# Optimization experiments

Hardware: AMD Instinct MI355X
Metric: run time of the kernel (lower is better)

The kernel has to match this reference:

```python
import jax, jax.numpy as jnp
import numpy as np

# SRU cell math (sru library v2.x, has_skip_term=False, identity activation):
#   U = x @ W  ->  split into (u0, u1, u2), each [L, B, H]
#   f_t = sigmoid(u1_t + v_f * c_{t-1} + b_f)
#   r_t = sigmoid(u2_t + v_r * c_{t-1} + b_r)
#   c_t = f_t * c_{t-1} + (1 - f_t) * u0_t
#   h_t = r_t * c_t            (no skip term, identity activation)

L, B, D, H, OUT = 512, 128, 128, 512, 5


def sru_layer(x, W, vc, b):
    # x: [L, B, Din]; W: [Din, 3H]; vc: [2H]; b: [2H]
    h = W.shape[1] // 3
    U = jnp.einsum('lbd,dk->lbk', x, W)          # [L, B, 3H]
    u0, u1, u2 = jnp.split(U, 3, axis=-1)
    vf, vr = vc[:h], vc[h:]
    bf, br = b[:h], b[h:]

    def step(c, u):
        u0t, u1t, u2t = u
        f = jax.nn.sigmoid(u1t + vf * c + bf)
        r = jax.nn.sigmoid(u2t + vr * c + br)
        c_new = f * c + (1.0 - f) * u0t
        return c_new, r * c_new

    c0 = jnp.zeros((x.shape[1], h), dtype=x.dtype)
    _, hs = jax.lax.scan(step, c0, (u0, u1, u2))  # hs: [L, B, H]
    return hs


def setup_inputs() -> dict:
    key = jax.random.key(0)
    ks = jax.random.split(key, 9)
    s_in = 1.0 / np.sqrt(D)
    s_h = 1.0 / np.sqrt(H)
    return {
        'x': jax.random.normal(ks[0], (L, B, D), jnp.float32),
        'W0': jax.random.normal(ks[1], (D, 3 * H), jnp.float32) * s_in,
        'v0': jax.random.normal(ks[2], (2 * H,), jnp.float32) * s_h,
        'b0': jnp.zeros((2 * H,), jnp.float32),
        'W1': jax.random.normal(ks[3], (H, 3 * H), jnp.float32) * s_h,
        'v1': jax.random.normal(ks[4], (2 * H,), jnp.float32) * s_h,
        'b1': jnp.zeros((2 * H,), jnp.float32),
        'fc_w': jax.random.normal(ks[5], (OUT, H), jnp.float32) * s_h,
        'fc_b': jnp.zeros((OUT,), jnp.float32),
    }


def reference(x, W0, v0, b0, W1, v1, b1, fc_w, fc_b):
    h1 = sru_layer(x, W0, v0, b0)    # [L, B, H]
    h2 = sru_layer(h1, W1, v1, b1)   # [L, B, H]
    # fc on last timestep
    return h2[-1] @ fc_w.T + fc_b    # [B, OUT]
```

## Files before the change

kernel.cpp:

```cpp
#include <hip/hip_runtime.h>
#include <math.h>

#define L_SEQ 512
#define BATCH 128
#define DIN   128
#define HID   512
#define NOUT  5

typedef unsigned short u16;
typedef unsigned int   u32;
typedef __attribute__((ext_vector_type(8))) short short8;
typedef __attribute__((ext_vector_type(4))) float f32x4;

__device__ __forceinline__ u16 f2bf(float x) {
  u32 u = __float_as_uint(x);
  return (u16)((u + 0x7fffu + ((u >> 16) & 1u)) >> 16);
}
__device__ __forceinline__ float bf2f(u16 s) {
  return __uint_as_float(((u32)s) << 16);
}
__device__ __forceinline__ void gload16(const void* g, void* l) {
  __builtin_amdgcn_global_load_lds(
      (const __attribute__((address_space(1))) u32*)g,
      (__attribute__((address_space(3))) u32*)l, 16, 0, 0);
}

#define R_AH 0
#define R_AL 8192
#define R_BH 16384
#define R_BL 20480
#define BUFSZ 24576u

__global__ __launch_bounds__(512, 1)
void gemm_bf16x3_8ph(const u16* __restrict__ Ah, const u16* __restrict__ Al,
                     const u16* __restrict__ Bh, const u16* __restrict__ Bl,
                     float* __restrict__ C, int N, int K, int NBX) {
  __shared__ u16 lds[3 * BUFSZ];

  const int NT = K >> 5;
  const int nwg = gridDim.x;
  int bid = blockIdx.x;
  if ((nwg & 7) == 0) {
    const int cpx = nwg >> 3;
    bid = (bid & 7) * cpx + (bid >> 3);
  }
  const int bx = bid % NBX, by = bid / NBX;

  const int tid = threadIdx.x;
  const int w = tid >> 6, lane = tid & 63;

  const int srow = lane >> 2;
  const int sslot = lane & 3;
  const int ra0 = w * 16 + srow;
  const int ra1 = 128 + ra0;
  const int swA0 = sslot ^ ((ra0 >> 1) & 3);
  const int swA1 = sslot ^ ((ra1 >> 1) & 3);
  const u16* pAh0 = Ah + (size_t)(by * 256 + ra0) * K + swA0 * 8;
  const u16* pAh1 = Ah + (size_t)(by * 256 + ra1) * K + swA1 * 8;
  const u16* pAl0 = Al + (size_t)(by * 256 + ra0) * K + swA0 * 8;
  const u16* pAl1 = Al + (size_t)(by * 256 + ra1) * K + swA1 * 8;
  const u16* pBh0 = Bh + (size_t)(bx * 128 + ra0) * K + swA0 * 8;
  const u16* pBl0 = Bl + (size_t)(bx * 128 + ra0) * K + swA0 * 8;
  const int dA0 = (w * 16) * 32;
  const int dA1 = (128 + w * 16) * 32;

  const int wm = w >> 1, wn = w & 1;
  const int frow = lane & 15, fsl = lane >> 4;
  int offA[4], offB[4];
#pragma unroll
  for (int i = 0; i < 4; ++i) {
    const int ra = wm * 64 + i * 16 + frow;
    offA[i] = ra * 32 + ((fsl ^ ((ra >> 1) & 3)) * 8);
    const int rb = wn * 64 + i * 16 + frow;
    offB[i] = rb * 32 + ((fsl ^ ((rb >> 1) & 3)) * 8);
  }

  f32x4 acc[4][4];
#pragma unroll
  for (int i = 0; i < 4; ++i)
#pragma unroll
    for (int j = 0; j < 4; ++j)
#pragma unroll
      for (int q = 0; q < 4; ++q) acc[i][j][q] = 0.f;

#define STAGE_A0(ks, stg) do { \
    gload16(pAh0 + (ks), &lds[(stg) + R_AH + dA0]); \
    gload16(pAl0 + (ks), &lds[(stg) + R_AL + dA0]); } while (0)
#define STAGE_A1(ks, stg) do { \
    gload16(pAh1 + (ks), &lds[(stg) + R_AH + dA1]); \
    gload16(pAl1 + (ks), &lds[(stg) + R_AL + dA1]); } while (0)
#define STAGE_BH(ks, stg) gload16(pBh0 + (ks), &lds[(stg) + R_BH + dA0])
#define STAGE_BL(ks, stg) gload16(pBl0 + (ks), &lds[(stg) + R_BL + dA0])

  STAGE_A0(0, 0u); STAGE_A1(0, 0u); STAGE_BH(0, 0u); STAGE_BL(0, 0u);
  STAGE_A0(32, BUFSZ); STAGE_A1(32, BUFSZ); STAGE_BH(32, BUFSZ); STAGE_BL(32, BUFSZ);
  asm volatile("s_waitcnt vmcnt(6)" ::: "memory");
  __builtin_amdgcn_s_barrier();

  unsigned bufs0 = 0, bufs1 = BUFSZ, bufs2 = 2 * BUFSZ;

#define PHASE(i, STAGE_STMT, TAIL) do { \
    const short8 a_h = *(const short8*)&lds[bufs0 + R_AH + offA[i]]; \
    const short8 a_l = *(const short8*)&lds[bufs0 + R_AL + offA[i]]; \
    STAGE_STMT; \
    __builtin_amdgcn_s_barrier(); \
    asm volatile("s_waitcnt lgkmcnt(0)" ::: "memory"); \
    __builtin_amdgcn_sched_barrier(0); \
    __builtin_amdgcn_s_setprio(1); \
    _Pragma("unroll") \
    for (int j = 0; j < 4; ++j) { \
      acc[i][j] = __builtin_amdgcn_mfma_f32_16x16x32_bf16(a_h, bh[j], acc[i][j], 0, 0, 0); \
      acc[i][j] = __builtin_amdgcn_mfma_f32_16x16x32_bf16(a_h, bl[j], acc[i][j], 0, 0, 0); \
      acc[i][j] = __builtin_amdgcn_mfma_f32_16x16x32_bf16(a_l, bh[j], acc[i][j], 0, 0, 0); \
    } \
    __builtin_amdgcn_s_setprio(0); \
    TAIL; \
    __builtin_amdgcn_s_barrier(); \
  } while (0)

  for (int t = 0; t < NT; ++t) {
    const int ks = (t + 2) * 32;
    const bool st = (t + 2) < NT;

    short8 bh[4], bl[4];
#pragma unroll
    for (int j = 0; j < 4; ++j) {
      bh[j] = *(const short8*)&lds[bufs0 + R_BH + offB[j]];
      bl[j] = *(const short8*)&lds[bufs0 + R_BL + offB[j]];
    }
    PHASE(0, if (st) STAGE_A0(ks, bufs2), );
    PHASE(1, if (st) STAGE_A1(ks, bufs2), );
    PHASE(2, if (st) STAGE_BH(ks, bufs2), );
    PHASE(3, if (st) STAGE_BL(ks, bufs2),
          if (t < NT - 2) { asm volatile("s_waitcnt vmcnt(6)" ::: "memory"); }
          else if (t == NT - 2) { asm volatile("s_waitcnt vmcnt(0)" ::: "memory"); });

    const unsigned tmp = bufs0; bufs0 = bufs1; bufs1 = bufs2; bufs2 = tmp;
  }
#undef PHASE
#undef STAGE_A0
#undef STAGE_A1
#undef STAGE_BH
#undef STAGE_BL

  const int crow0 = by * 256 + wm * 64 + (lane >> 4) * 4;
  const int ccol0 = bx * 128 + wn * 64 + (lane & 15);
#pragma unroll
  for (int i = 0; i < 4; ++i)
#pragma unroll
    for (int j = 0; j < 4; ++j) {
      float* cp = C + (size_t)(crow0 + i * 16) * N + ccol0 + j * 16;
#pragma unroll
      for (int q = 0; q < 4; ++q) cp[(size_t)q * N] = acc[i][j][q];
    }
}

__global__ __launch_bounds__(256)
void split4_f32(const float* __restrict__ in, u16* __restrict__ hi,
                u16* __restrict__ lo, int n4) {
  const int i = blockIdx.x * 256 + threadIdx.x;
  if (i >= n4) return;
  const float4 v = ((const float4*)in)[i];
  u16 h0 = f2bf(v.x), h1 = f2bf(v.y), h2 = f2bf(v.z), h3 = f2bf(v.w);
  u16 l0 = f2bf(v.x - bf2f(h0)), l1 = f2bf(v.y - bf2f(h1));
  u16 l2 = f2bf(v.z - bf2f(h2)), l3 = f2bf(v.w - bf2f(h3));
  uint2 hp, lp;
  hp.x = (u32)h0 | ((u32)h1 << 16); hp.y = (u32)h2 | ((u32)h3 << 16);
  lp.x = (u32)l0 | ((u32)l1 << 16); lp.y = (u32)l2 | ((u32)l3 << 16);
  ((uint2*)hi)[i] = hp;
  ((uint2*)lo)[i] = lp;
}

__global__ __launch_bounds__(256)
void split_w_t(const float* __restrict__ W, u16* __restrict__ Th,
               u16* __restrict__ Tl, int K, int N) {
  const int idx = blockIdx.x * 256 + threadIdx.x;
  if (idx >= K * N) return;
  const int k = idx / N, n = idx - k * N;
  const float x = W[idx];
  const u16 h = f2bf(x);
  Th[(size_t)n * K + k] = h;
  Tl[(size_t)n * K + k] = f2bf(x - bf2f(h));
}

__global__ __launch_bounds__(256)
void zero_f32(float* __restrict__ p, int n) {
  const int i = blockIdx.x * 256 + threadIdx.x;
  if (i < n) p[i] = 0.f;
}

__device__ __forceinline__ float sig(float x) { return 1.f / (1.f + __expf(-x)); }

__global__ __launch_bounds__(256)
void sru_scan0_chunk(const float* __restrict__ U, const float* __restrict__ v,
                     const float* __restrict__ bias, u16* __restrict__ h1h,
                     u16* __restrict__ h1l, float* __restrict__ cstate, int Tc) {
  const int j = blockIdx.x * 256 + threadIdx.x;
  const int b = j >> 9, h = j & (HID - 1);
  const float vf = v[h], vr = v[HID + h];
  const float bf = bias[h], br = bias[HID + h];

  const float* p = U + (size_t)b * (3 * HID) + h;
  const size_t sT = (size_t)BATCH * 3 * HID;
  u16* ph = h1h + (size_t)b * HID + h;
  u16* pl = h1l + (size_t)b * HID + h;
  const size_t sH = (size_t)BATCH * HID;

  float c = cstate[j];
  float cu[12];
#pragma unroll
  for (int q = 0; q < 4; ++q) {
    cu[3 * q + 0] = p[q * sT];
    cu[3 * q + 1] = p[q * sT + HID];
    cu[3 * q + 2] = p[q * sT + 2 * HID];
  }
  const int NG = Tc >> 2;
  for (int g = 0; g < NG; ++g) {
    float nx[12];
    const bool has = (g + 1 < NG);
    if (has) {
      const float* pn = p + 4 * sT;
#pragma unroll
      for (int q = 0; q < 4; ++q) {
        nx[3 * q + 0] = pn[q * sT];
        nx[3 * q + 1] = pn[q * sT + HID];
        nx[3 * q + 2] = pn[q * sT + 2 * HID];
      }
    }
#pragma unroll
    for (int q = 0; q < 4; ++q) {
      const float u0 = cu[3 * q], u1 = cu[3 * q + 1], u2 = cu[3 * q + 2];
      const float f = sig(u1 + vf * c + bf);
      const float r = sig(u2 + vr * c + br);
      c = f * c + (1.f - f) * u0;
      const float hv = r * c;
      const u16 hh = f2bf(hv);
      ph[(size_t)(g * 4 + q) * sH] = hh;
      pl[(size_t)(g * 4 + q) * sH] = f2bf(hv - bf2f(hh));
    }
    p += 4 * sT;
    if (has) {
#pragma unroll
      for (int i = 0; i < 12; ++i) cu[i] = nx[i];
    }
  }
  cstate[j] = c;
}

__global__ __launch_bounds__(256)
void sru_scan1_chunk(const float* __restrict__ U, const float* __restrict__ v,
                     const float* __restrict__ bias, float* __restrict__ cstate,
                     float* __restrict__ hlast, int Tc, int lastT) {
  const int j = blockIdx.x * 256 + threadIdx.x;
  const int b = j >> 9, h = j & (HID - 1);
  const float vf = v[h], vr = v[HID + h];
  const float bf = bias[h], br = bias[HID + h];

  const float* p = U + (size_t)b * (3 * HID) + h;
  const size_t sT = (size_t)BATCH * 3 * HID;

  float c = cstate[j];
  float cu[8];
#pragma unroll
  for (int q = 0; q < 4; ++q) {
    cu[2 * q + 0] = p[q * sT];
    cu[2 * q + 1] = p[q * sT + HID];
  }
  const int NG = Tc >> 2;
  for (int g = 0; g < NG; ++g) {
    float nx[8];
    const bool has = (g + 1 < NG);
    if (has) {
      const float* pn = p + 4 * sT;
#pragma unroll
      for (int q = 0; q < 4; ++q) {
        nx[2 * q + 0] = pn[q * sT];
        nx[2 * q + 1] = pn[q * sT + HID];
      }
    }
#pragma unroll
    for (int q = 0; q < 4; ++q) {
      const float u0 = cu[2 * q], u1 = cu[2 * q + 1];
      const float f = sig(u1 + vf * c + bf);
      const float cn = f * c + (1.f - f) * u0;
      if (g * 4 + q == lastT) {
        const float u2 = p[q * sT + 2 * HID];
        const float r = sig(u2 + vr * c + br);
        hlast[j] = r * cn;
      }
      c = cn;
    }
    p += 4 * sT;
    if (has) {
#pragma unroll
      for (int i = 0; i < 8; ++i) cu[i] = nx[i];
    }
  }
  cstate[j] = c;
}

__global__ __launch_bounds__(256)
void fc_head(const float* __restrict__ h, const float* __restrict__ w,
             const float* __restrict__ bias, float* __restrict__ out) {
  const int gid = blockIdx.x * 256 + threadIdx.x;
  const int wv = gid >> 6, lane = threadIdx.x & 63;
  if (wv >= BATCH * NOUT) return;
  const int b = wv / NOUT, o = wv % NOUT;
  float s = 0.f;
#pragma unroll
  for (int k = lane; k < HID; k += 64)
    s += h[(size_t)b * HID + k] * w[(size_t)o * HID + k];
#pragma unroll
  for (int off = 32; off > 0; off >>= 1) s += __shfl_down(s, off);
  if (lane == 0) out[(size_t)b * NOUT + o] = s + bias[o];
}

extern "C" void kernel_launch(void* const* d_in, const int* in_sizes, int n_in,
                              void* d_out, int out_size, void* d_ws, size_t ws_size,
                              hipStream_t stream) {
  const float* x   = (const float*)d_in[0];
  const float* W0  = (const float*)d_in[1];
  const float* v0  = (const float*)d_in[2];
  const float* b0  = (const float*)d_in[3];
  const float* W1  = (const float*)d_in[4];
  const float* v1  = (const float*)d_in[5];
  const float* b1  = (const float*)d_in[6];
  const float* fcw = (const float*)d_in[7];
  const float* fcb = (const float*)d_in[8];
  float* out = (float*)d_out;

  const size_t nX = (size_t)L_SEQ * BATCH * DIN;
  const size_t nW0 = (size_t)DIN * 3 * HID;
  const size_t nW1 = (size_t)HID * 3 * HID;

  int Tc = 128;
  for (;;) {
    size_t f32e = (size_t)Tc * BATCH * 3 * HID + 3 * (size_t)BATCH * HID;
    size_t u16e = 2 * nX + 2 * (size_t)Tc * BATCH * HID + 2 * nW0 + 2 * nW1;
    if (f32e * 4 + u16e * 2 + 1024 <= ws_size || Tc <= 8) break;
    Tc >>= 1;
  }
  const int NC = L_SEQ / Tc;
  const int Mc = Tc * BATCH;

  float* U0c = (float*)d_ws;
  float* c0  = U0c + (size_t)Mc * 3 * HID;
  float* c1  = c0 + (size_t)BATCH * HID;
  float* h2  = c1 + (size_t)BATCH * HID;
  u16* xs_h  = (u16*)(h2 + (size_t)BATCH * HID);
  u16* xs_l  = xs_h + nX;
  u16* h1_h  = xs_l + nX;
  u16* h1_l  = h1_h + (size_t)Mc * HID;
  u16* w0t_h = h1_l + (size_t)Mc * HID;
  u16* w0t_l = w0t_h + nW0;
  u16* w1t_h = w0t_l + nW0;
  u16* w1t_l = w1t_h + nW1;

  const int scan_grid = (BATCH * HID) / 256;
  const int fc_grid = (BATCH * NOUT * 64 + 255) / 256;
  const int grid_full = (Mc / 256) * 12;
  const int grid_01   = (Mc / 256) * 8;

  zero_f32<<<(2 * BATCH * HID) / 256, 256, 0, stream>>>(c0, 2 * BATCH * HID);
  split4_f32<<<(int)(nX / 4 + 255) / 256, 256, 0, stream>>>(x, xs_h, xs_l, (int)(nX / 4));
  split_w_t<<<(int)(nW0 + 255) / 256, 256, 0, stream>>>(W0, w0t_h, w0t_l, DIN, 3 * HID);
  split_w_t<<<(int)(nW1 + 255) / 256, 256, 0, stream>>>(W1, w1t_h, w1t_l, HID, 3 * HID);

  for (int ch = 0; ch < NC; ++ch) {
    const bool last = (ch == NC - 1);
    const size_t xoff = (size_t)ch * Tc * BATCH * DIN;
    gemm_bf16x3_8ph<<<grid_full, 512, 0, stream>>>(
        xs_h + xoff, xs_l + xoff, w0t_h, w0t_l, U0c, 3 * HID, DIN, 12);
    sru_scan0_chunk<<<scan_grid, 256, 0, stream>>>(U0c, v0, b0, h1_h, h1_l, c0, Tc);
    gemm_bf16x3_8ph<<<last ? grid_full : grid_01, 512, 0, stream>>>(
        h1_h, h1_l, w1t_h, w1t_l, U0c, 3 * HID, HID, last ? 12 : 8);
    sru_scan1_chunk<<<scan_grid, 256, 0, stream>>>(
        U0c, v1, b1, c1, h2, Tc, last ? Tc - 1 : -1);
  }
  fc_head<<<fc_grid, 256, 0, stream>>>(h2, fcw, fcb, out);
}
```

Baseline: 712.5 us.

## Enlarge GEMM tile to 256x256 with double-buffered LDS and drop zero kernel

Rewrites the split-bf16 GEMM to compute 256x256 output tiles per workgroup instead of 256x128. Each wave now holds an 8x4 accumulator block, and the kernel uses a two-stage LDS buffer in place of three stages. The larger tile halves the grid and raises operand reuse per loaded byte. In exchange it costs more accumulator registers (launch bounds now ask for 2 blocks) and gives a shallower prefetch pipeline. The separate zero-init kernel is also removed: the scan kernels now start from c=0 on the first chunk through a flag.

```diff
diff --git a/kernel.cpp b/kernel.cpp
--- a/kernel.cpp
+++ b/kernel.cpp
@@ -25,17 +25,13 @@
       (__attribute__((address_space(3))) u32*)l, 16, 0, 0);
 }
 
-#define R_AH 0
-#define R_AL 8192
-#define R_BH 16384
-#define R_BL 20480
-#define BUFSZ 24576u
-
-__global__ __launch_bounds__(512, 1)
-void gemm_bf16x3_8ph(const u16* __restrict__ Ah, const u16* __restrict__ Al,
-                     const u16* __restrict__ Bh, const u16* __restrict__ Bl,
-                     float* __restrict__ C, int N, int K, int NBX) {
-  __shared__ u16 lds[3 * BUFSZ];
+#define BUFSZ 32768u
+
+__global__ __launch_bounds__(512, 2)
+void gemm_bf16x3_v2(const u16* __restrict__ Ah, const u16* __restrict__ Al,
+                    const u16* __restrict__ Bh, const u16* __restrict__ Bl,
+                    float* __restrict__ C, int N, int K, int NBX) {
+  __shared__ u16 lds[2 * BUFSZ];
 
   const int NT = K >> 5;
   const int nwg = gridDim.x;
@@ -48,105 +44,126 @@
 
   const int tid = threadIdx.x;
   const int w = tid >> 6, lane = tid & 63;
-
-  const int srow = lane >> 2;
-  const int sslot = lane & 3;
-  const int ra0 = w * 16 + srow;
-  const int ra1 = 128 + ra0;
-  const int swA0 = sslot ^ ((ra0 >> 1) & 3);
-  const int swA1 = sslot ^ ((ra1 >> 1) & 3);
-  const u16* pAh0 = Ah + (size_t)(by * 256 + ra0) * K + swA0 * 8;
-  const u16* pAh1 = Ah + (size_t)(by * 256 + ra1) * K + swA1 * 8;
-  const u16* pAl0 = Al + (size_t)(by * 256 + ra0) * K + swA0 * 8;
-  const u16* pAl1 = Al + (size_t)(by * 256 + ra1) * K + swA1 * 8;
-  const u16* pBh0 = Bh + (size_t)(bx * 128 + ra0) * K + swA0 * 8;
-  const u16* pBl0 = Bl + (size_t)(bx * 128 + ra0) * K + swA0 * 8;
-  const int dA0 = (w * 16) * 32;
-  const int dA1 = (128 + w * 16) * 32;
-
-  const int wm = w >> 1, wn = w & 1;
+  const int wm = w >> 2, wn = w & 3;
+
+  const int r16 = lane >> 2, sl = lane & 3;
+  const int bB0 = wn * 64 + wm * 32;
+  const int aB0 = wm * 128 + wn * 16;
+
+  const int rB0 = bB0 + r16,      rB1 = bB0 + 16 + r16;
+  const int rA0 = aB0 + r16,      rA1 = aB0 + 64 + r16;
+  const u16* pB0h = Bh + (size_t)(bx * 256 + rB0) * K + ((sl ^ ((rB0 >> 1) & 3)) * 8);
+  const u16* pB0l = Bl + (size_t)(bx * 256 + rB0) * K + ((sl ^ ((rB0 >> 1) & 3)) * 8);
+  const u16* pB1h = Bh + (size_t)(bx * 256 + rB1) * K + ((sl ^ ((rB1 >> 1) & 3)) * 8);
+  const u16* pB1l = Bl + (size_t)(bx * 256 + rB1) * K + ((sl ^ ((rB1 >> 1) & 3)) * 8);
+  const u16* pA0h = Ah + (size_t)(by * 256 + rA0) * K + ((sl ^ ((rA0 >> 1) & 3)) * 8);
+  const u16* pA0l = Al + (size_t)(by * 256 + rA0) * K + ((sl ^ ((rA0 >> 1) & 3)) * 8);
+  const u16* pA1h = Ah + (size_t)(by * 256 + rA1) * K + ((sl ^ ((rA1 >> 1) & 3)) * 8);
+  const u16* pA1l = Al + (size_t)(by * 256 + rA1) * K + ((sl ^ ((rA1 >> 1) & 3)) * 8);
+  const int dB = 16384 + bB0 * 32;
+  const int dA = aB0 * 32;
+
+#define STAGE_P0(ks, sb) do { gload16(pB0h + (ks), &lds[(sb) + dB]); \
+                              gload16(pB0l + (ks), &lds[(sb) + dB + 8192]); } while (0)
+#define STAGE_P1(ks, sb) do { gload16(pB1h + (ks), &lds[(sb) + dB + 512]); \
+                              gload16(pB1l + (ks), &lds[(sb) + dB + 8704]); } while (0)
+#define STAGE_P2(ks, sb) do { gload16(pA0h + (ks), &lds[(sb) + dA]); \
+                              gload16(pA0l + (ks), &lds[(sb) + dA + 8192]); } while (0)
+#define STAGE_P3(ks, sb) do { gload16(pA1h + (ks), &lds[(sb) + dA + 2048]); \
+                              gload16(pA1l + (ks), &lds[(sb) + dA + 10240]); } while (0)
+
   const int frow = lane & 15, fsl = lane >> 4;
-  int offA[4], offB[4];
-#pragma unroll
-  for (int i = 0; i < 4; ++i) {
-    const int ra = wm * 64 + i * 16 + frow;
+  int offA[8], offB[4];
+#pragma unroll
+  for (int i = 0; i < 8; ++i) {
+    const int ra = wm * 128 + i * 16 + frow;
     offA[i] = ra * 32 + ((fsl ^ ((ra >> 1) & 3)) * 8);
-    const int rb = wn * 64 + i * 16 + frow;
-    offB[i] = rb * 32 + ((fsl ^ ((rb >> 1) & 3)) * 8);
-  }
-
-  f32x4 acc[4][4];
-#pragma unroll
-  for (int i = 0; i < 4; ++i)
+  }
+#pragma unroll
+  for (int j = 0; j < 4; ++j) {
+    const int rb = wn * 64 + j * 16 + frow;
+    offB[j] = 16384 + rb * 32 + ((fsl ^ ((rb >> 1) & 3)) * 8);
+  }
+
+  f32x4 acc[8][4];
+#pragma unroll
+  for (int i = 0; i < 8; ++i)
 #pragma unroll
     for (int j = 0; j < 4; ++j)
 #pragma unroll
       for (int q = 0; q < 4; ++q) acc[i][j][q] = 0.f;
 
-#define STAGE_A0(ks, stg) do { \
-    gload16(pAh0 + (ks), &lds[(stg) + R_AH + dA0]); \
-    gload16(pAl0 + (ks), &lds[(stg) + R_AL + dA0]); } while (0)
-#define STAGE_A1(ks, stg) do { \
-    gload16(pAh1 + (ks), &lds[(stg) + R_AH + dA1]); \
-    gload16(pAl1 + (ks), &lds[(stg) + R_AL + dA1]); } while (0)
-#define STAGE_BH(ks, stg) gload16(pBh0 + (ks), &lds[(stg) + R_BH + dA0])
-#define STAGE_BL(ks, stg) gload16(pBl0 + (ks), &lds[(stg) + R_BL + dA0])
-
-  STAGE_A0(0, 0u); STAGE_A1(0, 0u); STAGE_BH(0, 0u); STAGE_BL(0, 0u);
-  STAGE_A0(32, BUFSZ); STAGE_A1(32, BUFSZ); STAGE_BH(32, BUFSZ); STAGE_BL(32, BUFSZ);
-  asm volatile("s_waitcnt vmcnt(6)" ::: "memory");
+  STAGE_P0(0, 0u); STAGE_P1(0, 0u); STAGE_P2(0, 0u); STAGE_P3(0, 0u);
+  asm volatile("s_waitcnt vmcnt(0)" ::: "memory");
   __builtin_amdgcn_s_barrier();
 
-  unsigned bufs0 = 0, bufs1 = BUFSZ, bufs2 = 2 * BUFSZ;
-
-#define PHASE(i, STAGE_STMT, TAIL) do { \
-    const short8 a_h = *(const short8*)&lds[bufs0 + R_AH + offA[i]]; \
-    const short8 a_l = *(const short8*)&lds[bufs0 + R_AL + offA[i]]; \
-    STAGE_STMT; \
+#define MFMA3(i, j, aa_h, aa_l) \
+    acc[i][j] = __builtin_amdgcn_mfma_f32_16x16x32_bf16(aa_h, bh[j], acc[i][j], 0, 0, 0); \
+    acc[i][j] = __builtin_amdgcn_mfma_f32_16x16x32_bf16(aa_h, bl[j], acc[i][j], 0, 0, 0); \
+    acc[i][j] = __builtin_amdgcn_mfma_f32_16x16x32_bf16(aa_l, bh[j], acc[i][j], 0, 0, 0)
+
+#define PHASE(p, STG, TAIL) do { \
+    const short8 ah0 = *(const short8*)&lds[cb + offA[2 * (p)]]; \
+    const short8 al0 = *(const short8*)&lds[cb + 8192 + offA[2 * (p)]]; \
+    const short8 ah1 = *(const short8*)&lds[cb + offA[2 * (p) + 1]]; \
+    const short8 al1 = *(const short8*)&lds[cb + 8192 + offA[2 * (p) + 1]]; \
+    STG; \
     __builtin_amdgcn_s_barrier(); \
     asm volatile("s_waitcnt lgkmcnt(0)" ::: "memory"); \
     __builtin_amdgcn_sched_barrier(0); \
     __builtin_amdgcn_s_setprio(1); \
     _Pragma("unroll") \
     for (int j = 0; j < 4; ++j) { \
-      acc[i][j] = __builtin_amdgcn_mfma_f32_16x16x32_bf16(a_h, bh[j], acc[i][j], 0, 0, 0); \
-      acc[i][j] = __builtin_amdgcn_mfma_f32_16x16x32_bf16(a_h, bl[j], acc[i][j], 0, 0, 0); \
-      acc[i][j] = __builtin_amdgcn_mfma_f32_16x16x32_bf16(a_l, bh[j], acc[i][j], 0, 0, 0); \
+      acc[2*(p)][j]   = __builtin_amdgcn_mfma_f32_16x16x32_bf16(ah0, bh[j], acc[2*(p)][j], 0, 0, 0); \
+      acc[2*(p)+1][j] = __builtin_amdgcn_mfma_f32_16x16x32_bf16(ah1, bh[j], acc[2*(p)+1][j], 0, 0, 0); \
+    } \
+    _Pragma("unroll") \
+    for (int j = 0; j < 4; ++j) { \
+      acc[2*(p)][j]   = __builtin_amdgcn_mfma_f32_16x16x32_bf16(ah0, bl[j], acc[2*(p)][j], 0, 0, 0); \
+      acc[2*(p)+1][j] = __builtin_amdgcn_mfma_f32_16x16x32_bf16(ah1, bl[j], acc[2*(p)+1][j], 0, 0, 0); \
+    } \
+    _Pragma("unroll") \
+    for (int j = 0; j < 4; ++j) { \
+      acc[2*(p)][j]   = __builtin_amdgcn_mfma_f32_16x16x32_bf16(al0, bh[j], acc[2*(p)][j], 0, 0, 0); \
+      acc[2*(p)+1][j] = __builtin_amdgcn_mfma_f32_16x16x32_bf16(al1, bh[j], acc[2*(p)+1][j], 0, 0, 0); \
     } \
     __builtin_amdgcn_s_setprio(0); \
     TAIL; \
     __builtin_amdgcn_s_barrier(); \
   } while (0)
 
+  int cb = 0;
   for (int t = 0; t < NT; ++t) {
-    const int ks = (t + 2) * 32;
-    const bool st = (t + 2) < NT;
+    const int ks = (t + 1) << 5;
+    const bool st = (t + 1) < NT;
+    const int sb = cb ^ (int)BUFSZ;
 
     short8 bh[4], bl[4];
 #pragma unroll
     for (int j = 0; j < 4; ++j) {
-      bh[j] = *(const short8*)&lds[bufs0 + R_BH + offB[j]];
-      bl[j] = *(const short8*)&lds[bufs0 + R_BL + offB[j]];
-    }
-    PHASE(0, if (st) STAGE_A0(ks, bufs2), );
-    PHASE(1, if (st) STAGE_A1(ks, bufs2), );
-    PHASE(2, if (st) STAGE_BH(ks, bufs2), );
-    PHASE(3, if (st) STAGE_BL(ks, bufs2),
-          if (t < NT - 2) { asm volatile("s_waitcnt vmcnt(6)" ::: "memory"); }
-          else if (t == NT - 2) { asm volatile("s_waitcnt vmcnt(0)" ::: "memory"); });
-
-    const unsigned tmp = bufs0; bufs0 = bufs1; bufs1 = bufs2; bufs2 = tmp;
+      bh[j] = *(const short8*)&lds[cb + offB[j]];
+      bl[j] = *(const short8*)&lds[cb + 8192 + offB[j]];
+    }
+    PHASE(0, if (st) STAGE_P0(ks, sb), );
+    PHASE(1, if (st) STAGE_P1(ks, sb),
+          if (st) { asm volatile("s_waitcnt vmcnt(4)" ::: "memory"); }
+          else    { asm volatile("s_waitcnt vmcnt(0)" ::: "memory"); });
+    PHASE(2, if (st) STAGE_P2(ks, sb), );
+    PHASE(3, if (st) STAGE_P3(ks, sb),
+          if (st) { asm volatile("s_waitcnt vmcnt(2)" ::: "memory"); });
+    cb = sb;
   }
 #undef PHASE
-#undef STAGE_A0
-#undef STAGE_A1
-#undef STAGE_BH
-#undef STAGE_BL
-
-  const int crow0 = by * 256 + wm * 64 + (lane >> 4) * 4;
-  const int ccol0 = bx * 128 + wn * 64 + (lane & 15);
-#pragma unroll
-  for (int i = 0; i < 4; ++i)
+#undef MFMA3
+#undef STAGE_P0
+#undef STAGE_P1
+#undef STAGE_P2
+#undef STAGE_P3
+
+  const int crow0 = by * 256 + wm * 128 + (lane >> 4) * 4;
+  const int ccol0 = bx * 256 + wn * 64 + (lane & 15);
+#pragma unroll
+  for (int i = 0; i < 8; ++i)
 #pragma unroll
     for (int j = 0; j < 4; ++j) {
       float* cp = C + (size_t)(crow0 + i * 16) * N + ccol0 + j * 16;
@@ -183,18 +200,13 @@
   Tl[(size_t)n * K + k] = f2bf(x - bf2f(h));
 }
 
-__global__ __launch_bounds__(256)
-void zero_f32(float* __restrict__ p, int n) {
-  const int i = blockIdx.x * 256 + threadIdx.x;
-  if (i < n) p[i] = 0.f;
-}
-
 __device__ __forceinline__ float sig(float x) { return 1.f / (1.f + __expf(-x)); }
 
 __global__ __launch_bounds__(256)
 void sru_scan0_chunk(const float* __restrict__ U, const float* __restrict__ v,
                      const float* __restrict__ bias, u16* __restrict__ h1h,
-                     u16* __restrict__ h1l, float* __restrict__ cstate, int Tc) {
+                     u16* __restrict__ h1l, float* __restrict__ cstate, int Tc,
+                     int init) {
   const int j = blockIdx.x * 256 + threadIdx.x;
   const int b = j >> 9, h = j & (HID - 1);
   const float vf = v[h], vr = v[HID + h];
@@ -206,7 +218,7 @@
   u16* pl = h1l + (size_t)b * HID + h;
   const size_t sH = (size_t)BATCH * HID;
 
-  float c = cstate[j];
+  float c = init ? 0.f : cstate[j];
   float cu[12];
 #pragma unroll
   for (int q = 0; q < 4; ++q) {
@@ -250,7 +262,7 @@
 __global__ __launch_bounds__(256)
 void sru_scan1_chunk(const float* __restrict__ U, const float* __restrict__ v,
                      const float* __restrict__ bias, float* __restrict__ cstate,
-                     float* __restrict__ hlast, int Tc, int lastT) {
+                     float* __restrict__ hlast, int Tc, int lastT, int init) {
   const int j = blockIdx.x * 256 + threadIdx.x;
   const int b = j >> 9, h = j & (HID - 1);
   const float vf = v[h], vr = v[HID + h];
@@ -259,7 +271,7 @@
   const float* p = U + (size_t)b * (3 * HID) + h;
   const size_t sT = (size_t)BATCH * 3 * HID;
 
-  float c = cstate[j];
+  float c = init ? 0.f : cstate[j];
   float cu[8];
 #pragma unroll
   for (int q = 0; q < 4; ++q) {
@@ -358,10 +370,9 @@
 
   const int scan_grid = (BATCH * HID) / 256;
   const int fc_grid = (BATCH * NOUT * 64 + 255) / 256;
-  const int grid_full = (Mc / 256) * 12;
-  const int grid_01   = (Mc / 256) * 8;
-
-  zero_f32<<<(2 * BATCH * HID) / 256, 256, 0, stream>>>(c0, 2 * BATCH * HID);
+  const int grid_full = (Mc / 256) * 6;
+  const int grid_01   = (Mc / 256) * 4;
+
   split4_f32<<<(int)(nX / 4 + 255) / 256, 256, 0, stream>>>(x, xs_h, xs_l, (int)(nX / 4));
   split_w_t<<<(int)(nW0 + 255) / 256, 256, 0, stream>>>(W0, w0t_h, w0t_l, DIN, 3 * HID);
   split_w_t<<<(int)(nW1 + 255) / 256, 256, 0, stream>>>(W1, w1t_h, w1t_l, HID, 3 * HID);
@@ -369,13 +380,14 @@
   for (int ch = 0; ch < NC; ++ch) {
     const bool last = (ch == NC - 1);
     const size_t xoff = (size_t)ch * Tc * BATCH * DIN;
-    gemm_bf16x3_8ph<<<grid_full, 512, 0, stream>>>(
-        xs_h + xoff, xs_l + xoff, w0t_h, w0t_l, U0c, 3 * HID, DIN, 12);
-    sru_scan0_chunk<<<scan_grid, 256, 0, stream>>>(U0c, v0, b0, h1_h, h1_l, c0, Tc);
-    gemm_bf16x3_8ph<<<last ? grid_full : grid_01, 512, 0, stream>>>(
-        h1_h, h1_l, w1t_h, w1t_l, U0c, 3 * HID, HID, last ? 12 : 8);
+    gemm_bf16x3_v2<<<grid_full, 512, 0, stream>>>(
+        xs_h + xoff, xs_l + xoff, w0t_h, w0t_l, U0c, 3 * HID, DIN, 6);
+    sru_scan0_chunk<<<scan_grid, 256, 0, stream>>>(U0c, v0, b0, h1_h, h1_l, c0, Tc,
+                                                   ch == 0);
+    gemm_bf16x3_v2<<<last ? grid_full : grid_01, 512, 0, stream>>>(
+        h1_h, h1_l, w1t_h, w1t_l, U0c, 3 * HID, HID, last ? 6 : 4);
     sru_scan1_chunk<<<scan_grid, 256, 0, stream>>>(
-        U0c, v1, b1, c1, h2, Tc, last ? Tc - 1 : -1);
+        U0c, v1, b1, c1, h2, Tc, last ? Tc - 1 : -1, ch == 0);
   }
   fc_head<<<fc_grid, 256, 0, stream>>>(h2, fcw, fcb, out);
 }
```

New measurement: 679.3 us. 4.7% less time.
